# Performance work log

Hardware: AMD Instinct MI355X
Metric: run time of the kernel (lower is better)

## Reference

```python
import math
import jax, jax.numpy as jnp
import numpy as np

N_NODES = 100000
N_EDGES = 1200000
N_BASIS = 20
HIDDEN = 50
SILU_NORM = 1.679  # e3nn normalize2mom constant for silu
LMAX_SH = 5
MID_LS = (0, 1, 2, 3, 4)          # middle = 1x0e+1x1o+1x2e+1x3o+1x4e (dim 25)
OUT_L = 2                          # out = 1x2e (dim 5)
TP2_PATHS = ((0, 2), (1, 1), (1, 3), (2, 0), (2, 2), (2, 4), (3, 1), (3, 3), (3, 5), (4, 2), (4, 4))
NUM_NEIGHBORS = 6


def _fact(n):
    return math.factorial(n)


def _cg(j1, m1, j2, m2, j3, m3):
    # Racah formula for Clebsch-Gordan coefficients (complex SH, Condon-Shortley).
    if m1 + m2 != m3:
        return 0.0
    pref = math.sqrt((2 * j3 + 1) * _fact(j1 + j2 - j3) * _fact(j1 - j2 + j3) * _fact(-j1 + j2 + j3) / _fact(j1 + j2 + j3 + 1))
    pref *= math.sqrt(_fact(j1 + m1) * _fact(j1 - m1) * _fact(j2 + m2) * _fact(j2 - m2) * _fact(j3 + m3) * _fact(j3 - m3))
    s = 0.0
    for k in range(j1 + j2 - j3 + 1):
        d = (k, j1 + j2 - j3 - k, j1 - m1 - k, j2 + m2 - k, j3 - j2 + m1 + k, j3 - j1 - m2 + k)
        if min(d) < 0:
            continue
        den = 1.0
        for q in d:
            den *= _fact(q)
        s += (-1.0) ** k / den
    return pref * s


def _u_real(l):
    # change of basis complex SH -> real SH, rows indexed by real m=-l..l
    U = np.zeros((2 * l + 1, 2 * l + 1), dtype=np.complex128)
    U[l, l] = 1.0
    rt2 = math.sqrt(2.0)
    for m in range(1, l + 1):
        U[l + m, l + m] = (-1.0) ** m / rt2
        U[l + m, l - m] = 1.0 / rt2
        U[l - m, l + m] = -1j * (-1.0) ** m / rt2
        U[l - m, l - m] = 1j / rt2
    return U


def _w3j_real(j1, j2, j3):
    # real-basis Wigner 3j tensor (real for even j1+j2+j3, which holds for all paths here)
    Wc = np.zeros((2 * j1 + 1, 2 * j2 + 1, 2 * j3 + 1), dtype=np.complex128)
    for m1 in range(-j1, j1 + 1):
        for m2 in range(-j2, j2 + 1):
            m3 = -(m1 + m2)
            if abs(m3) <= j3:
                Wc[j1 + m1, j2 + m2, j3 + m3] = (-1.0) ** (j1 - j2 - m3) / math.sqrt(2 * j3 + 1) * _cg(j1, m1, j2, m2, j3, -m3)
    U1, U2, U3 = _u_real(j1).conj(), _u_real(j2).conj(), _u_real(j3).conj()
    Wr = np.einsum('abc,ia,jb,kc->ijk', Wc, U1, U2, U3)
    return np.ascontiguousarray(Wr.real.astype(np.float32))


W3J_TP1 = {l: _w3j_real(0, l, l) for l in MID_LS}
W3J_TP2 = {p: _w3j_real(p[0], p[1], OUT_L) for p in TP2_PATHS}


def spherical_harmonics(vec):
    # vec [E,3] -> component-normalized real SH for l=0..5, concatenated [E,36]
    r = jnp.sqrt(jnp.sum(vec * vec, axis=1))
    x, y, z = vec[:, 0] / r, vec[:, 1] / r, vec[:, 2] / r
    phi = jnp.arctan2(y, x)
    s = jnp.sqrt(jnp.clip(1.0 - z * z, 0.0, 1.0))
    # associated Legendre P[l][m] without Condon-Shortley phase
    P = [[None] * (l + 1) for l in range(LMAX_SH + 1)]
    P[0][0] = jnp.ones_like(z)
    for m in range(1, LMAX_SH + 1):
        P[m][m] = (2 * m - 1) * s * P[m - 1][m - 1]
    for m in range(0, LMAX_SH):
        P[m + 1][m] = (2 * m + 1) * z * P[m][m]
    for l in range(2, LMAX_SH + 1):
        for m in range(0, l - 1):
            P[l][m] = ((2 * l - 1) * z * P[l - 1][m] - (l - 1 + m) * P[l - 2][m]) / (l - m)
    blocks = []
    for l in range(LMAX_SH + 1):
        comps = []
        for m in range(-l, l + 1):
            am = abs(m)
            c = math.sqrt((2 * l + 1) * _fact(l - am) / _fact(l + am)) * (math.sqrt(2.0) if m != 0 else 1.0)
            if m < 0:
                ang = jnp.sin(am * phi)
            elif m > 0:
                ang = jnp.cos(am * phi)
            else:
                ang = jnp.ones_like(phi)
            comps.append(c * P[l][am] * ang)
        blocks.append(jnp.stack(comps, axis=1))
    return jnp.concatenate(blocks, axis=1)


def soft_one_hot(d):
    # e3nn soft_one_hot_linspace(basis='smooth_finite', cutoff=True), start=0, end=3
    values = jnp.linspace(0.0, 3.0, N_BASIS + 2)
    step = values[1] - values[0]
    values = values[1:-1]
    diff = (d[:, None] - values[None, :]) / step

    def sus(t):
        safe = jnp.where(t > 0, t, 1.0)
        return jnp.where(t > 0, jnp.exp(-1.0 / safe), 0.0)

    return 1.14136 * math.exp(2.0) * sus(diff + 1.0) * sus(1.0 - diff)


def tp1(x_scalar, sh, w):
    # FullyConnectedTensorProduct(1x0e, sh, middle) with external per-edge weights w [E,5]
    outs = []
    for i, l in enumerate(MID_LS):
        W = W3J_TP1[l][0]                       # [2l+1, 2l+1]
        alpha = math.sqrt(2 * l + 1)            # sqrt(dim_out / fan_in), fan_in = 1
        shl = sh[:, l * l:(l + 1) * (l + 1)]
        outs.append(alpha * w[:, i:i + 1] * x_scalar * (shl @ W))
    return jnp.concatenate(outs, axis=1)        # [E, 25]


def tp2(feat, sh, w):
    # FullyConnectedTensorProduct(middle, sh, 1x2e) with internal weights w [11]
    alpha = math.sqrt((2 * OUT_L + 1) / len(TP2_PATHS))
    out = jnp.zeros((feat.shape[0], 2 * OUT_L + 1), dtype=feat.dtype)
    for p, (l1, l2) in enumerate(TP2_PATHS):
        W = W3J_TP2[(l1, l2)]                   # [2l1+1, 2l2+1, 5]
        f = feat[:, l1 * l1:(l1 + 1) * (l1 + 1)]
        s = sh[:, l2 * l2:(l2 + 1) * (l2 + 1)]
        tmp = jnp.einsum('ei,ijk->ejk', f, W)
        out = out + (alpha * w[p]) * jnp.einsum('ejk,ej->ek', tmp, s)
    return out                                   # [E, 5]


def _forward(x, pos, edge_index, mlp_w1, mlp_w2, tp2_w):
    N = pos.shape[0]
    edge_from = edge_index[:, 0]
    edge_to = edge_index[:, 1]
    Co = jnp.argmax(jnp.bincount(edge_to, length=N))          # torch.mode(edge_to)
    edge_vec = pos[edge_to] - pos[edge_from]
    sh = spherical_harmonics(edge_vec)                         # [E, 36]
    dist = jnp.linalg.norm(edge_vec, axis=1)
    emb = soft_one_hot(dist)                                   # [E, 20]
    h = jax.nn.silu(emb @ mlp_w1 / math.sqrt(N_BASIS)) * SILU_NORM
    tp_w = h @ mlp_w2 / math.sqrt(HIDDEN)                      # [E, 5]
    feat = tp1(x[edge_to], sh, tp_w)                           # [E, 25]
    node = jax.ops.segment_sum(feat, edge_from, num_segments=N) / math.sqrt(float(NUM_NEIGHBORS))
    feat2 = tp2(node[edge_to], sh, tp2_w)                      # [E, 5]
    node2 = jax.ops.segment_sum(feat2, edge_from, num_segments=N)
    return node2[Co]                                           # [5]


def setup_inputs():
    N, E = N_NODES, N_EDGES
    key = jax.random.key(0)
    k = jax.random.split(key, 7)
    pos = 1.5 * jax.random.normal(k[0], (N, 3), dtype=jnp.float32)
    x = jax.random.normal(k[1], (N, 1), dtype=jnp.float32)
    ef = jax.random.randint(k[2], (E,), 0, N, dtype=jnp.int32)
    off = jax.random.randint(k[3], (E,), 1, N, dtype=jnp.int32)
    et = (ef + off) % N                                        # no self loops -> nonzero edge_vec
    edge_index = jnp.stack([ef, et], axis=1)
    mlp_w1 = jax.random.normal(k[4], (N_BASIS, HIDDEN), dtype=jnp.float32)
    mlp_w2 = jax.random.normal(k[5], (HIDDEN, len(MID_LS)), dtype=jnp.float32)
    tp2_w = jax.random.normal(k[6], (len(TP2_PATHS),), dtype=jnp.float32)
    return {'x': x, 'pos': pos, 'edge_index': edge_index, 'mlp_w1': mlp_w1, 'mlp_w2': mlp_w2, 'tp2_w': tp2_w}


def reference(x, pos, edge_index, mlp_w1, mlp_w2, tp2_w):
    return _forward(x, pos, edge_index, mlp_w1, mlp_w2, tp2_w)
```

## Files before the change

### kernel.cpp

```cpp
#include <hip/hip_runtime.h>
#include <math.h>

#define CAP 2048
#define HALF_MAX 12544


struct WSPtrs {
  unsigned* slices;
  int* flag;
  unsigned long long* key;
  int* co_count;
  int* s_count;
  int* co_edges;
  float* node_acc;
  float* w3j1;
  float* w3j2;
  size_t fb_zero_bytes;
  size_t total_bytes;
};

__host__ __device__ inline WSPtrs make_ws(char* ws, int N, int half, int C, int fb){
  WSPtrs p;
  size_t o = 0;
  p.slices   = (unsigned*)(ws + o);
  o += fb ? (size_t)N * 4 : (size_t)C * 2 * half * 4;
  p.flag     = (int*)(ws + o); o += (size_t)N * 4;
  o = (o + 7) & ~(size_t)7;
  p.key      = (unsigned long long*)(ws + o); o += 8;
  p.co_count = (int*)(ws + o); o += 4;
  p.s_count  = (int*)(ws + o); o += 4;
  p.co_edges = (int*)(ws + o); o += (size_t)CAP * 4;
  p.node_acc = (float*)(ws + o); o += (size_t)CAP * 25 * 4;
  p.fb_zero_bytes = o;
  p.w3j1     = (float*)(ws + o); o += 165 * 4;
  p.w3j2     = (float*)(ws + o); o += 1915 * 4;
  p.total_bytes = o;
  return p;
}


__device__ double cg_coef_lut(int j1,int m1,int j2,int m2,int j3,int m3, const double* __restrict__ fact){
  if (m1 + m2 != m3) return 0.0;
  double pref = sqrt((2.0*j3+1.0) * fact[j1+j2-j3] * fact[j1-j2+j3] * fact[-j1+j2+j3]
                     / fact[j1+j2+j3+1]);
  pref *= sqrt(fact[j1+m1]*fact[j1-m1]*fact[j2+m2]*fact[j2-m2]*fact[j3+m3]*fact[j3-m3]);
  double s = 0.0;
  for (int k = 0; k <= j1+j2-j3; ++k){
    int d2 = j1-m1-k, d3 = j2+m2-k, d4 = j3-j2+m1+k, d5 = j3-j1-m2+k;
    if (d2 < 0 || d3 < 0 || d4 < 0 || d5 < 0) continue;
    double den = fact[k]*fact[j1+j2-j3-k]*fact[d2]*fact[d3]*fact[d4]*fact[d5];
    s += ((k & 1) ? -1.0 : 1.0) / den;
  }
  return pref * s;
}

__device__ double wigner_c_val_lut(int j1,int j2,int j3,int m1,int m2,int m3, const double* __restrict__ fact){
  if (m1+m2+m3 != 0) return 0.0;
  int e = j1 - j2 - m3;
  double sign = (e & 1) ? -1.0 : 1.0;
  return sign / sqrt(2.0*j3+1.0) * cg_coef_lut(j1,m1,j2,m2,j3,-m3,fact);
}

__device__ int conjU_row(int l, int i, int* cols, double* re, double* im){
  int mr = i - l;
  const double irt2 = 0.70710678118654752440;
  if (mr == 0){ cols[0]=l; re[0]=1.0; im[0]=0.0; return 1; }
  int m = mr > 0 ? mr : -mr;
  double sgn = (m & 1) ? -1.0 : 1.0;
  if (mr > 0){
    cols[0]=l+m; re[0]=sgn*irt2; im[0]=0.0;
    cols[1]=l-m; re[1]=irt2;     im[1]=0.0;
  } else {
    cols[0]=l+m; re[0]=0.0; im[0]= sgn*irt2;
    cols[1]=l-m; re[1]=0.0; im[1]=-irt2;
  }
  return 2;
}

__device__ void wigner_entry(int entry, const double* __restrict__ sfact,
                             float* __restrict__ w3j1, float* __restrict__ w3j2){
  if (entry >= 165 + 1915) return;
  int j1, j2, j3, ii, jj, kk;
  float* dst;
  if (entry < 165){
    const int l1off[5] = {0,1,10,35,84};
    int l = 4;
    for (int q = 1; q < 5; ++q) if (entry < l1off[q]){ l = q-1; break; }
    int t = entry - l1off[l];
    int n = 2*l+1;
    j1 = 0; j2 = l; j3 = l;
    ii = 0; jj = t / n; kk = t % n;
    dst = &w3j1[entry];
  } else {
    int t2 = entry - 165;
    const int pl1[11]  = {0,1,1,2,2,2,3,3,3,4,4};
    const int pl2[11]  = {2,1,3,0,2,4,1,3,5,2,4};
    const int poff[11] = {0,25,70,175,200,325,550,655,900,1285,1510};
    int p = 10;
    for (int q = 1; q < 11; ++q) if (t2 < poff[q]){ p = q-1; break; }
    int t = t2 - poff[p];
    j1 = pl1[p]; j2 = pl2[p]; j3 = 2;
    int n2q = 2*j2+1;
    ii = t / (n2q*5); int rem = t % (n2q*5); jj = rem / 5; kk = rem % 5;
    dst = &w3j2[t2];
  }
  int c1[2], c2[2], c3[2];
  double r1[2], i1[2], r2[2], i2[2], r3[2], i3[2];
  int n1 = conjU_row(j1, ii, c1, r1, i1);
  int n2 = conjU_row(j2, jj, c2, r2, i2);
  int n3 = conjU_row(j3, kk, c3, r3, i3);
  double acc = 0.0;
  for (int combo = 0; combo < 8; ++combo){
    int a = (combo >> 2) & 1, b = (combo >> 1) & 1, c = combo & 1;
    if (a >= n1 || b >= n2 || c >= n3) continue;
    int m1 = c1[a]-j1, m2 = c2[b]-j2, m3 = c3[c]-j3;
    if (m1 + m2 + m3 != 0) continue;
    double wc = wigner_c_val_lut(j1,j2,j3,m1,m2,m3,sfact);
    if (wc == 0.0) continue;
    double pr = r1[a]*r2[b] - i1[a]*i2[b];
    double pi = r1[a]*i2[b] + i1[a]*r2[b];
    acc += wc * (pr*r3[c] - pi*i3[c]);
  }
  *dst = (float)acc;
}


__device__ void compute_sh36f(float ex, float ey, float ez, float* __restrict__ sh){
  float r = sqrtf(ex*ex + ey*ey + ez*ez);
  float x = ex/r, y = ey/r, z = ez/r;
  float t = 1.0f - z*z;
  t = t < 0.0f ? 0.0f : (t > 1.0f ? 1.0f : t);
  float s = sqrtf(t);
  float rxy = sqrtf(x*x + y*y);
  float c1, s1;
  if (rxy > 1e-30f){ c1 = x/rxy; s1 = y/rxy; } else { c1 = 1.0f; s1 = 0.0f; }
  float cm[6], sm[6];
  cm[0] = 1.0f; sm[0] = 0.0f;
  for (int m = 1; m <= 5; ++m){
    cm[m] = cm[m-1]*c1 - sm[m-1]*s1;
    sm[m] = sm[m-1]*c1 + cm[m-1]*s1;
  }
  float P[6][6];
  P[0][0] = 1.0f;
  for (int m=1;m<=5;m++) P[m][m] = (float)(2*m-1)*s*P[m-1][m-1];
  for (int m=0;m<5;m++)  P[m+1][m] = (float)(2*m+1)*z*P[m][m];
  for (int l=2;l<=5;l++)
    for (int m=0;m<=l-2;m++)
      P[l][m] = ((float)(2*l-1)*z*P[l-1][m] - (float)(l-1+m)*P[l-2][m])/(float)(l-m);
  const float rt2 = 1.41421356237309504880f;
  for (int l=0;l<=5;l++){
    for (int m=-l;m<=l;m++){
      int am = m < 0 ? -m : m;
      float ratio = 1.0f;
      for (int k = l-am+1; k <= l+am; ++k) ratio *= (float)k;
      float c = sqrtf((float)(2*l+1)/ratio);
      if (m != 0) c *= rt2;
      float ang = (m < 0) ? sm[am] : ((m > 0) ? cm[am] : 1.0f);
      sh[l*l + m + l] = c * P[l][am] * ang;
    }
  }
}

__device__ void feat_edge(int f, int t, const int* __restrict__ flag,
                          const float* __restrict__ pos, const float* __restrict__ x,
                          const float* __restrict__ w1, const float* __restrict__ w2,
                          const float* w3j1, float* __restrict__ node_acc){
  int slot = flag[f] - 1;
  if (slot < 0 || slot >= CAP) return;

  float ex = pos[3*t+0] - pos[3*f+0];
  float ey = pos[3*t+1] - pos[3*f+1];
  float ez = pos[3*t+2] - pos[3*f+2];
  float sh[36];
  compute_sh36f(ex,ey,ez,sh);
  float d = sqrtf(ex*ex+ey*ey+ez*ez);

  float emb[20];
  const float step = 3.0f/21.0f;
  const float cemb = 1.14136f * 7.38905609893065f;
  for (int jb=0;jb<20;jb++){
    float v = step*(float)(jb+1);
    float diff = (d - v)/step;
    float a = diff + 1.0f, b = 1.0f - diff;
    float sa = (a > 0.0f) ? __expf(-1.0f/a) : 0.0f;
    float sb = (b > 0.0f) ? __expf(-1.0f/b) : 0.0f;
    emb[jb] = cemb * sa * sb;
  }
  float tw[5] = {0,0,0,0,0};
  const float is20 = 0.22360679774997896964f;
  const float is50 = 0.14142135623730950488f;
  for (int kk=0;kk<50;kk++){
    float z = 0.0f;
    for (int jb=0;jb<20;jb++) z += emb[jb]*w1[jb*50+kk];
    z *= is20;
    float hk = (z / (1.0f + __expf(-z))) * 1.679f;
    for (int i=0;i<5;i++) tw[i] += hk * w2[kk*5+i];
  }
  for (int i=0;i<5;i++) tw[i] *= is50;

  float xs = x[t];
  const int w1off[5] = {0,1,10,35,84};
  const float alphal[5] = {1.0f, 1.73205080756887729353f, 2.23606797749978969641f,
                           2.64575131106459059050f, 3.0f};
  int fo = 0;
  for (int l=0;l<5;l++){
    int nl = 2*l+1;
    float scale = alphal[l] * tw[l] * xs;
    for (int kq=0;kq<nl;kq++){
      float acc = 0.0f;
      for (int jq=0;jq<nl;jq++) acc += sh[l*l+jq]*w3j1[w1off[l]+jq*nl+kq];
      atomicAdd(&node_acc[slot*25 + fo + kq], scale*acc);
    }
    fo += nl;
  }
}

__device__ void tp2_task(int e, int p, const int2* __restrict__ ei, const int* __restrict__ flag,
                         const float* __restrict__ pos, const float* __restrict__ node_acc,
                         const float* w3j2, const float* __restrict__ tp2w,
                         float* __restrict__ acc){
  const float inv_sqrt6 = 0.40824829046386301637f;
  const float alpha2    = 0.67419986246324704794f;
  const int pl1[11]  = {0,1,1,2,2,2,3,3,3,4,4};
  const int pl2[11]  = {2,1,3,0,2,4,1,3,5,2,4};
  const int poff[11] = {0,25,70,175,200,325,550,655,900,1285,1510};
  int2 fe = ei[e];
  int f = fe.x, t = fe.y;
  int slot = flag[t] - 1;
  if (slot < 0 || slot >= CAP) return;
  float ex = pos[3*t+0] - pos[3*f+0];
  float ey = pos[3*t+1] - pos[3*f+1];
  float ez = pos[3*t+2] - pos[3*f+2];
  float sh[36];
  compute_sh36f(ex,ey,ez,sh);
  int l1 = pl1[p], l2 = pl2[p], n1 = 2*l1+1, n2 = 2*l2+1;
  const float* W = w3j2 + poff[p];
  float wp = alpha2 * tp2w[p];
  for (int i=0;i<n1;i++){
    float fi = node_acc[slot*25 + l1*l1 + i] * inv_sqrt6;
    for (int j=0;j<n2;j++){
      float fs = wp*fi*sh[l2*l2+j];
      const float* Wij = W + (i*n2+j)*5;
      for (int k=0;k<5;k++) acc[k] += fs*Wij[k];
    }
  }
}


__global__ __launch_bounds__(1024)
void count_w3j_kernel(const int2* __restrict__ ei, unsigned* __restrict__ slices,
                      int* __restrict__ flag, unsigned long long* __restrict__ key,
                      int* __restrict__ co_count, int* __restrict__ s_count,
                      float* __restrict__ node_acc,
                      float* __restrict__ w3j1, float* __restrict__ w3j2,
                      int N, int half, int E, int C){
  __shared__ double sfact[16];
  __shared__ unsigned hist[HALF_MAX];
  if (threadIdx.x == 0){
    double rr = 1.0;
    sfact[0] = 1.0;
    for (int i = 1; i < 16; ++i){ rr *= (double)i; sfact[i] = rr; }
  }
  for (int i = threadIdx.x; i < half; i += blockDim.x) hist[i] = 0;
  __syncthreads();

  int gtid = blockIdx.x*blockDim.x + threadIdx.x;
  int gsize = gridDim.x*blockDim.x;

  if (gtid < 2080) wigner_entry(gtid, sfact, w3j1, w3j2);

  for (int i = gtid; i < N; i += gsize) flag[i] = 0;
  for (int i = gtid; i < CAP*25; i += gsize) node_acc[i] = 0.0f;
  if (gtid == 0){ *key = 0ull; *co_count = 0; *s_count = 0; }

  int c = blockIdx.x >> 1;
  int r = blockIdx.x & 1;
  int wbase = r * half;
  size_t e0 = (size_t)c * (size_t)E / (size_t)C;
  size_t e1 = (size_t)(c+1) * (size_t)E / (size_t)C;
  for (size_t e = e0 + threadIdx.x; e < e1; e += blockDim.x){
    int v = ei[e].y;
    int lw = (v >> 2) - wbase;
    if (lw >= 0 && lw < half)
      atomicAdd(&hist[lw], 1u << ((v & 3) * 8));
  }
  __syncthreads();

  unsigned* dst = slices + (size_t)(c*2 + r) * half;
  for (int i = threadIdx.x; i < half; i += blockDim.x) dst[i] = hist[i];
}

__global__ void count_fb_kernel(const int2* __restrict__ ei, unsigned* __restrict__ counts,
                                float* __restrict__ w3j1, float* __restrict__ w3j2, int E){
  __shared__ double sfact[16];
  if (threadIdx.x == 0){
    double rr = 1.0;
    sfact[0] = 1.0;
    for (int i = 1; i < 16; ++i){ rr *= (double)i; sfact[i] = rr; }
  }
  __syncthreads();
  int tid = blockIdx.x*blockDim.x + threadIdx.x;
  if (tid < 2080) wigner_entry(tid, sfact, w3j1, w3j2);
  if (tid < E) atomicAdd(&counts[ei[tid].y], 1u);
}

__global__ void argmax_kernel(const unsigned* __restrict__ slices, unsigned long long* __restrict__ key,
                              int N, int Nw, int half, int C, int fb){
  __shared__ unsigned long long sred[256];
  int w = blockIdx.x*blockDim.x + threadIdx.x;
  unsigned long long best = 0;
  if (fb){
    if (w < N)
      best = ((unsigned long long)slices[w] << 32) | (unsigned)(N-1-w);
  } else if (w < Nw){
    int r = (w >= half) ? 1 : 0;
    int lw = w - r*half;
    unsigned sum = 0;
    for (int c = 0; c < C; ++c)
      sum += slices[(size_t)(c*2 + r) * half + lw];
    for (int q = 0; q < 4; ++q){
      int idx = w*4 + q;
      if (idx < N){
        unsigned cnt = (sum >> (q*8)) & 0xffu;
        unsigned long long k = ((unsigned long long)cnt << 32) | (unsigned)(N-1-idx);
        if (k > best) best = k;
      }
    }
  }
  sred[threadIdx.x] = best;
  __syncthreads();
  for (int s = 128; s > 0; s >>= 1){
    if (threadIdx.x < s){
      unsigned long long o = sred[threadIdx.x+s];
      if (o > sred[threadIdx.x]) sred[threadIdx.x] = o;
    }
    __syncthreads();
  }
  if (threadIdx.x == 0) atomicMax(key, sred[0]);
}

__global__ void find_co_kernel(const int2* __restrict__ ei, const unsigned long long* __restrict__ key,
                               int* __restrict__ flag, int* __restrict__ co_count,
                               int* __restrict__ s_count, int* __restrict__ co_edges, int N, int E){
  int e = blockIdx.x*blockDim.x + threadIdx.x;
  if (e >= E) return;
  int Co = N - 1 - (int)(unsigned int)(*key & 0xffffffffull);
  int2 fe = ei[e];
  if (fe.x != Co) return;
  int p = atomicAdd(co_count, 1);
  if (p < CAP) co_edges[p] = e;
  int v = fe.y;
  if (atomicCAS(&flag[v], 0, -1) == 0){
    int slot = atomicAdd(s_count, 1);
    flag[v] = (slot < CAP) ? (slot + 1) : 0;
  }
}

__global__ void collect_feat_kernel(const int2* __restrict__ ei, const int* __restrict__ flag,
                                    const float* __restrict__ pos, const float* __restrict__ x,
                                    const float* __restrict__ w1, const float* __restrict__ w2,
                                    const float* __restrict__ w3j1g, float* __restrict__ node_acc,
                                    int E){
  __shared__ float sw3j1[165];
  for (int i = threadIdx.x; i < 165; i += blockDim.x) sw3j1[i] = w3j1g[i];
  __syncthreads();
  int e = blockIdx.x*blockDim.x + threadIdx.x;
  if (e >= E) return;
  int2 fe = ei[e];
  if (flag[fe.x] > 0)
    feat_edge(fe.x, fe.y, flag, pos, x, w1, w2, sw3j1, node_acc);
}

__global__ void out_kernel(const int2* __restrict__ ei, const int* __restrict__ flag,
                           const float* __restrict__ pos, const float* __restrict__ node_acc,
                           const float* __restrict__ w3j2g, const float* __restrict__ tp2w,
                           const int* __restrict__ co_count, const int* __restrict__ co_edges,
                           float* __restrict__ out){
  __shared__ float sw3j2[1915];
  __shared__ float red[256*5];
  for (int i = threadIdx.x; i < 1915; i += blockDim.x) sw3j2[i] = w3j2g[i];
  __syncthreads();
  float acc[5] = {0,0,0,0,0};
  int n = *co_count; if (n > CAP) n = CAP;
  int tasks = n * 11;
  for (int task = threadIdx.x; task < tasks; task += blockDim.x)
    tp2_task(co_edges[task/11], task%11, ei, flag, pos, node_acc, sw3j2, tp2w, acc);
  for (int k=0;k<5;k++) red[threadIdx.x*5+k] = acc[k];
  __syncthreads();
  if (threadIdx.x < 5){
    float s = 0.0f;
    for (int t2=0;t2<256;t2++) s += red[t2*5+threadIdx.x];
    out[threadIdx.x] = s;
  }
}


extern "C" void kernel_launch(void* const* d_in, const int* in_sizes, int n_in,
                              void* d_out, int out_size, void* d_ws, size_t ws_size,
                              hipStream_t stream){
  const int2*  ei2  = (const int2*)d_in[2];
  const float* xp   = (const float*)d_in[0];
  const float* posp = (const float*)d_in[1];
  const float* w1p  = (const float*)d_in[3];
  const float* w2p  = (const float*)d_in[4];
  const float* tpwp = (const float*)d_in[5];
  float* outp = (float*)d_out;
  char* wsp = (char*)d_ws;
  int N = in_sizes[0];
  int E = in_sizes[2] / 2;
  int Nw = (N + 3) >> 2;
  int half = (Nw + 1) >> 1;

  int fb = (half > HALF_MAX) ? 1 : 0;
  int C = 0;
  if (!fb){
    for (int cand = 128; cand >= 8; cand >>= 1){
      WSPtrs p = make_ws(wsp, N, half, cand, 0);
      if (p.total_bytes + 64 <= ws_size){ C = cand; break; }
    }
    if (C == 0) fb = 1;
  }
  WSPtrs P = make_ws(wsp, N, half, fb ? 1 : C, fb);

  int eblocks = (E + 255)/256;
  if (fb){
    hipMemsetAsync(d_ws, 0, P.fb_zero_bytes, stream);
    count_fb_kernel<<<eblocks, 256, 0, stream>>>(ei2, P.slices, P.w3j1, P.w3j2, E);
  } else {
    count_w3j_kernel<<<2*C, 1024, 0, stream>>>(ei2, P.slices, P.flag, P.key,
                                               P.co_count, P.s_count, P.node_acc,
                                               P.w3j1, P.w3j2, N, half, E, C);
  }
  int ablocks = fb ? (N + 255)/256 : (Nw + 255)/256;
  argmax_kernel     <<<ablocks, 256, 0, stream>>>(P.slices, P.key, N, Nw, half, C, fb);
  find_co_kernel    <<<eblocks, 256, 0, stream>>>(ei2, P.key, P.flag, P.co_count, P.s_count,
                                                  P.co_edges, N, E);
  collect_feat_kernel<<<eblocks, 256, 0, stream>>>(ei2, P.flag, posp, xp, w1p, w2p, P.w3j1,
                                                   P.node_acc, E);
  out_kernel        <<<1, 256, 0, stream>>>(ei2, P.flag, posp, P.node_acc, P.w3j2, tpwp,
                                            P.co_count, P.co_edges, outp);
}
```

Baseline: 166.5 us.

## Fuse neighbor feature collection with second tensor product, drop node accumulator

```diff
diff --git a/kernel.cpp b/kernel.cpp
--- a/kernel.cpp
+++ b/kernel.cpp
@@ -10,9 +10,7 @@
   int* flag;
   unsigned long long* key;
   int* co_count;
-  int* s_count;
   int* co_edges;
-  float* node_acc;
   float* w3j1;
   float* w3j2;
   size_t fb_zero_bytes;
@@ -27,11 +25,9 @@
   p.flag     = (int*)(ws + o); o += (size_t)N * 4;
   o = (o + 7) & ~(size_t)7;
   p.key      = (unsigned long long*)(ws + o); o += 8;
-  p.co_count = (int*)(ws + o); o += 4;
-  p.s_count  = (int*)(ws + o); o += 4;
+  p.co_count = (int*)(ws + o); o += 8;
+  p.fb_zero_bytes = o;
   p.co_edges = (int*)(ws + o); o += (size_t)CAP * 4;
-  p.node_acc = (float*)(ws + o); o += (size_t)CAP * 25 * 4;
-  p.fb_zero_bytes = o;
   p.w3j1     = (float*)(ws + o); o += 165 * 4;
   p.w3j2     = (float*)(ws + o); o += 1915 * 4;
   p.total_bytes = o;
@@ -161,13 +157,10 @@
   }
 }
 
-__device__ void feat_edge(int f, int t, const int* __restrict__ flag,
-                          const float* __restrict__ pos, const float* __restrict__ x,
-                          const float* __restrict__ w1, const float* __restrict__ w2,
-                          const float* w3j1, float* __restrict__ node_acc){
-  int slot = flag[f] - 1;
-  if (slot < 0 || slot >= CAP) return;
-
+__device__ void feat_edge_reg(int f, int t,
+                              const float* __restrict__ pos, const float* __restrict__ x,
+                              const float* __restrict__ w1, const float* __restrict__ w2,
+                              const float* w3j1, float* __restrict__ feat){
   float ex = pos[3*t+0] - pos[3*f+0];
   float ey = pos[3*t+1] - pos[3*f+1];
   float ez = pos[3*t+2] - pos[3*f+2];
@@ -209,14 +202,13 @@
     for (int kq=0;kq<nl;kq++){
       float acc = 0.0f;
       for (int jq=0;jq<nl;jq++) acc += sh[l*l+jq]*w3j1[w1off[l]+jq*nl+kq];
-      atomicAdd(&node_acc[slot*25 + fo + kq], scale*acc);
+      feat[fo + kq] = scale*acc;
     }
     fo += nl;
   }
 }
 
-__device__ void tp2_task(int e, int p, const int2* __restrict__ ei, const int* __restrict__ flag,
-                         const float* __restrict__ pos, const float* __restrict__ node_acc,
+__device__ void tp2_feat(const float* __restrict__ feat, const float* __restrict__ sh,
                          const float* w3j2, const float* __restrict__ tp2w,
                          float* __restrict__ acc){
   const float inv_sqrt6 = 0.40824829046386301637f;
@@ -224,24 +216,17 @@
   const int pl1[11]  = {0,1,1,2,2,2,3,3,3,4,4};
   const int pl2[11]  = {2,1,3,0,2,4,1,3,5,2,4};
   const int poff[11] = {0,25,70,175,200,325,550,655,900,1285,1510};
-  int2 fe = ei[e];
-  int f = fe.x, t = fe.y;
-  int slot = flag[t] - 1;
-  if (slot < 0 || slot >= CAP) return;
-  float ex = pos[3*t+0] - pos[3*f+0];
-  float ey = pos[3*t+1] - pos[3*f+1];
-  float ez = pos[3*t+2] - pos[3*f+2];
-  float sh[36];
-  compute_sh36f(ex,ey,ez,sh);
-  int l1 = pl1[p], l2 = pl2[p], n1 = 2*l1+1, n2 = 2*l2+1;
-  const float* W = w3j2 + poff[p];
-  float wp = alpha2 * tp2w[p];
-  for (int i=0;i<n1;i++){
-    float fi = node_acc[slot*25 + l1*l1 + i] * inv_sqrt6;
-    for (int j=0;j<n2;j++){
-      float fs = wp*fi*sh[l2*l2+j];
-      const float* Wij = W + (i*n2+j)*5;
-      for (int k=0;k<5;k++) acc[k] += fs*Wij[k];
+  for (int p=0;p<11;p++){
+    int l1 = pl1[p], l2 = pl2[p], n1 = 2*l1+1, n2 = 2*l2+1;
+    const float* W = w3j2 + poff[p];
+    float wp = alpha2 * tp2w[p];
+    for (int i=0;i<n1;i++){
+      float fi = feat[l1*l1+i] * inv_sqrt6;
+      for (int j=0;j<n2;j++){
+        float fs = wp*fi*sh[l2*l2+j];
+        const float* Wij = W + (i*n2+j)*5;
+        for (int k=0;k<5;k++) acc[k] += fs*Wij[k];
+      }
     }
   }
 }
@@ -250,8 +235,7 @@
 __global__ __launch_bounds__(1024)
 void count_w3j_kernel(const int2* __restrict__ ei, unsigned* __restrict__ slices,
                       int* __restrict__ flag, unsigned long long* __restrict__ key,
-                      int* __restrict__ co_count, int* __restrict__ s_count,
-                      float* __restrict__ node_acc,
+                      int* __restrict__ co_count, float* __restrict__ out,
                       float* __restrict__ w3j1, float* __restrict__ w3j2,
                       int N, int half, int E, int C){
   __shared__ double sfact[16];
@@ -268,10 +252,11 @@
   int gsize = gridDim.x*blockDim.x;
 
   if (gtid < 2080) wigner_entry(gtid, sfact, w3j1, w3j2);
-
   for (int i = gtid; i < N; i += gsize) flag[i] = 0;
-  for (int i = gtid; i < CAP*25; i += gsize) node_acc[i] = 0.0f;
-  if (gtid == 0){ *key = 0ull; *co_count = 0; *s_count = 0; }
+  if (gtid == 0){
+    *key = 0ull; *co_count = 0;
+    for (int k = 0; k < 5; ++k) out[k] = 0.0f;
+  }
 
   int c = blockIdx.x >> 1;
   int r = blockIdx.x & 1;
@@ -291,7 +276,8 @@
 }
 
 __global__ void count_fb_kernel(const int2* __restrict__ ei, unsigned* __restrict__ counts,
-                                float* __restrict__ w3j1, float* __restrict__ w3j2, int E){
+                                float* __restrict__ w3j1, float* __restrict__ w3j2,
+                                float* __restrict__ out, int E){
   __shared__ double sfact[16];
   if (threadIdx.x == 0){
     double rr = 1.0;
@@ -301,6 +287,7 @@
   __syncthreads();
   int tid = blockIdx.x*blockDim.x + threadIdx.x;
   if (tid < 2080) wigner_entry(tid, sfact, w3j1, w3j2);
+  if (tid == 0) for (int k = 0; k < 5; ++k) out[k] = 0.0f;
   if (tid < E) atomicAdd(&counts[ei[tid].y], 1u);
 }
 
@@ -341,7 +328,7 @@
 
 __global__ void find_co_kernel(const int2* __restrict__ ei, const unsigned long long* __restrict__ key,
                                int* __restrict__ flag, int* __restrict__ co_count,
-                               int* __restrict__ s_count, int* __restrict__ co_edges, int N, int E){
+                               int* __restrict__ co_edges, int N, int E){
   int e = blockIdx.x*blockDim.x + threadIdx.x;
   if (e >= E) return;
   int Co = N - 1 - (int)(unsigned int)(*key & 0xffffffffull);
@@ -349,49 +336,47 @@
   if (fe.x != Co) return;
   int p = atomicAdd(co_count, 1);
   if (p < CAP) co_edges[p] = e;
-  int v = fe.y;
-  if (atomicCAS(&flag[v], 0, -1) == 0){
-    int slot = atomicAdd(s_count, 1);
-    flag[v] = (slot < CAP) ? (slot + 1) : 0;
-  }
-}
-
-__global__ void collect_feat_kernel(const int2* __restrict__ ei, const int* __restrict__ flag,
-                                    const float* __restrict__ pos, const float* __restrict__ x,
-                                    const float* __restrict__ w1, const float* __restrict__ w2,
-                                    const float* __restrict__ w3j1g, float* __restrict__ node_acc,
-                                    int E){
+  flag[fe.y] = 1;
+}
+
+__global__ void feat_tp2_kernel(const int2* __restrict__ ei, const int* __restrict__ flag,
+                                const float* __restrict__ pos, const float* __restrict__ x,
+                                const float* __restrict__ w1, const float* __restrict__ w2,
+                                const float* __restrict__ w3j1g, const float* __restrict__ w3j2g,
+                                const float* __restrict__ tp2w,
+                                const int* __restrict__ co_count, const int* __restrict__ co_edges,
+                                float* __restrict__ out, int E){
   __shared__ float sw3j1[165];
-  for (int i = threadIdx.x; i < 165; i += blockDim.x) sw3j1[i] = w3j1g[i];
-  __syncthreads();
+  __shared__ float sw3j2[1915];
   int e = blockIdx.x*blockDim.x + threadIdx.x;
-  if (e >= E) return;
-  int2 fe = ei[e];
-  if (flag[fe.x] > 0)
-    feat_edge(fe.x, fe.y, flag, pos, x, w1, w2, sw3j1, node_acc);
-}
-
-__global__ void out_kernel(const int2* __restrict__ ei, const int* __restrict__ flag,
-                           const float* __restrict__ pos, const float* __restrict__ node_acc,
-                           const float* __restrict__ w3j2g, const float* __restrict__ tp2w,
-                           const int* __restrict__ co_count, const int* __restrict__ co_edges,
-                           float* __restrict__ out){
-  __shared__ float sw3j2[1915];
-  __shared__ float red[256*5];
+  int2 fe = make_int2(0, 0);
+  int has = 0;
+  if (e < E){ fe = ei[e]; has = (flag[fe.x] > 0); }
+  if (__syncthreads_or(has) == 0) return;
+
+  for (int i = threadIdx.x; i < 165; i += blockDim.x)  sw3j1[i] = w3j1g[i];
   for (int i = threadIdx.x; i < 1915; i += blockDim.x) sw3j2[i] = w3j2g[i];
   __syncthreads();
+  if (!has) return;
+
+  float feat[25];
+  feat_edge_reg(fe.x, fe.y, pos, x, w1, w2, sw3j1, feat);
+
+  int nC = *co_count; if (nC > CAP) nC = CAP;
   float acc[5] = {0,0,0,0,0};
-  int n = *co_count; if (n > CAP) n = CAP;
-  int tasks = n * 11;
-  for (int task = threadIdx.x; task < tasks; task += blockDim.x)
-    tp2_task(co_edges[task/11], task%11, ei, flag, pos, node_acc, sw3j2, tp2w, acc);
-  for (int k=0;k<5;k++) red[threadIdx.x*5+k] = acc[k];
-  __syncthreads();
-  if (threadIdx.x < 5){
-    float s = 0.0f;
-    for (int t2=0;t2<256;t2++) s += red[t2*5+threadIdx.x];
-    out[threadIdx.x] = s;
-  }
+  int wrote = 0;
+  for (int c = 0; c < nC; ++c){
+    int2 ce = ei[co_edges[c]];
+    if (ce.y != fe.x) continue;
+    float sh[36];
+    compute_sh36f(pos[3*ce.y+0] - pos[3*ce.x+0],
+                  pos[3*ce.y+1] - pos[3*ce.x+1],
+                  pos[3*ce.y+2] - pos[3*ce.x+2], sh);
+    tp2_feat(feat, sh, sw3j2, tp2w, acc);
+    wrote = 1;
+  }
+  if (wrote)
+    for (int k = 0; k < 5; ++k) atomicAdd(&out[k], acc[k]);
 }
 
 
@@ -425,18 +410,16 @@
   int eblocks = (E + 255)/256;
   if (fb){
     hipMemsetAsync(d_ws, 0, P.fb_zero_bytes, stream);
-    count_fb_kernel<<<eblocks, 256, 0, stream>>>(ei2, P.slices, P.w3j1, P.w3j2, E);
+    count_fb_kernel<<<eblocks, 256, 0, stream>>>(ei2, P.slices, P.w3j1, P.w3j2, outp, E);
   } else {
     count_w3j_kernel<<<2*C, 1024, 0, stream>>>(ei2, P.slices, P.flag, P.key,
-                                               P.co_count, P.s_count, P.node_acc,
-                                               P.w3j1, P.w3j2, N, half, E, C);
+                                               P.co_count, outp, P.w3j1, P.w3j2,
+                                               N, half, E, C);
   }
   int ablocks = fb ? (N + 255)/256 : (Nw + 255)/256;
-  argmax_kernel     <<<ablocks, 256, 0, stream>>>(P.slices, P.key, N, Nw, half, C, fb);
-  find_co_kernel    <<<eblocks, 256, 0, stream>>>(ei2, P.key, P.flag, P.co_count, P.s_count,
-                                                  P.co_edges, N, E);
-  collect_feat_kernel<<<eblocks, 256, 0, stream>>>(ei2, P.flag, posp, xp, w1p, w2p, P.w3j1,
-                                                   P.node_acc, E);
-  out_kernel        <<<1, 256, 0, stream>>>(ei2, P.flag, posp, P.node_acc, P.w3j2, tpwp,
-                                            P.co_count, P.co_edges, outp);
-}
+  argmax_kernel  <<<ablocks, 256, 0, stream>>>(P.slices, P.key, N, Nw, half, C, fb);
+  find_co_kernel <<<eblocks, 256, 0, stream>>>(ei2, P.key, P.flag, P.co_count, P.co_edges, N, E);
+  feat_tp2_kernel<<<eblocks, 256, 0, stream>>>(ei2, P.flag, posp, xp, w1p, w2p,
+                                               P.w3j1, P.w3j2, tpwp,
+                                               P.co_count, P.co_edges, outp, E);
+}
```

After: 443.0 us. 2.66x slower.
